# Kernel tuning notes

Measured on AMD Instinct MI355X. Metric: run time of the kernel, lower is better.

## Reference

```python
import jax, jax.numpy as jnp
import numpy as np

IN_F = 128
OUT_F = 64
ALPHA = 0.2  # LeakyReLU slope for attention logits
NEG_INF = -9e15


def setup_inputs() -> dict:
    key = jax.random.key(0)
    k1, k2, k3, k4 = jax.random.split(key, 4)
    B, N = 4, 2048
    h = jax.random.normal(k1, (B, N, IN_F), dtype=jnp.float32)
    adj = jax.random.randint(k2, (B, N, N), 0, 2, dtype=jnp.int32)
    # xavier_uniform with gain=1.414
    def xavier(k, shape, gain=1.414):
        fan_in, fan_out = shape[0], shape[1]
        bound = gain * np.sqrt(6.0 / (fan_in + fan_out))
        return jax.random.uniform(k, shape, jnp.float32, -bound, bound)
    W = xavier(k3, (IN_F, OUT_F))
    a = xavier(k4, (2 * OUT_F, 1))
    return {"h": h, "adj": adj, "W": W, "a": a}


def reference(h, adj, W, a):
    # Wh: [B, N, F_out]
    Wh = jnp.einsum("bnf,fo->bno", h, W)
    # e_ij = LeakyReLU(a_left . Wh_i + a_right . Wh_j), avoiding the
    # O(N^2 * 2F) concatenated tensor the torch code materializes.
    a_l = a[:OUT_F, 0]   # [F_out]
    a_r = a[OUT_F:, 0]   # [F_out]
    e_l = Wh @ a_l       # [B, N]
    e_r = Wh @ a_r       # [B, N]
    e = jax.nn.leaky_relu(e_l[:, :, None] + e_r[:, None, :], ALPHA)  # [B,N,N]
    masked = jnp.where(adj > 0, e, NEG_INF)
    attention = jax.nn.softmax(masked, axis=2)
    # dropout p=0.0 (eval-mode / deterministic) -> identity
    h_prime = jax.nn.leaky_relu(jnp.einsum("bij,bjo->bio", attention, Wh), 0.01)
    return (h_prime, attention)
```

## Files before the change

### kernel.cpp

```cpp
#include <hip/hip_runtime.h>

#define NN 2048
#define BB 4
#define IN_F 128
#define OUT_F 64
#define NEG_INF -9000000000000000.0f

typedef __attribute__((ext_vector_type(8))) short short8;
typedef __attribute__((ext_vector_type(4))) float f32x4;

__device__ __forceinline__ ushort f2bf(float f) {
  uint u = __float_as_uint(f);
  uint r = (u + 0x7fffu + ((u >> 16) & 1u)) >> 16;
  return (ushort)r;
}

__global__ __launch_bounds__(64) void wh_el_er_kernel(
    const float* __restrict__ h, const float* __restrict__ W,
    const float* __restrict__ a, ushort* __restrict__ Whbf,
    float* __restrict__ el, float* __restrict__ er) {
  int row = blockIdx.x;
  int o = threadIdx.x;
  const float* hr = h + (size_t)row * IN_F;
  float wh = 0.f;
  #pragma unroll 8
  for (int f = 0; f < IN_F; ++f) wh += hr[f] * W[f * OUT_F + o];
  Whbf[(size_t)row * OUT_F + o] = f2bf(wh);
  float vl = wh * a[o];
  float vr = wh * a[OUT_F + o];
  #pragma unroll
  for (int d = 32; d > 0; d >>= 1) {
    vl += __shfl_down(vl, d);
    vr += __shfl_down(vr, d);
  }
  if (o == 0) { el[row] = vl; er[row] = vr; }
}

__global__ __launch_bounds__(256) void transpose_kernel(
    const ushort* __restrict__ Whbf, ushort* __restrict__ WhbfT) {
  __shared__ uint tile[64][65];
  int b = blockIdx.x >> 5;
  int j0 = (blockIdx.x & 31) << 6;
  int t = threadIdx.x;
  int o = t & 63, jg = t >> 6;
  #pragma unroll
  for (int m = 0; m < 16; ++m) {
    int jj = jg * 16 + m;
    tile[jj][o] = (uint)Whbf[((size_t)(b * NN + j0 + jj)) * OUT_F + o];
  }
  __syncthreads();
  int oo = t >> 2, grp = t & 3;
  uint out[8];
  #pragma unroll
  for (int m = 0; m < 16; m += 2) {
    uint u0 = tile[grp * 16 + m][oo];
    uint u1 = tile[grp * 16 + m + 1][oo];
    out[m >> 1] = u0 | (u1 << 16);
  }
  uint4* dst = (uint4*)(WhbfT + ((size_t)(b * OUT_F + oo)) * NN + j0 + grp * 16);
  dst[0] = *(uint4*)&out[0];
  dst[1] = *(uint4*)&out[4];
}

__global__ __launch_bounds__(512, 4) void attn_kernel(
    const int* __restrict__ adj, const ushort* __restrict__ WhbfT,
    const float* __restrict__ el, const float* __restrict__ er,
    float* __restrict__ attn_out, float* __restrict__ hprime) {
  __shared__ __align__(16) char pbuf[16 * 4096];
  __shared__ float red[4][16][16];

  int blk = blockIdx.x;
  int b = blk >> 7;
  int i0 = (blk & 127) << 4;
  int tid = threadIdx.x;
  int wave = tid >> 6, lane = tid & 63;

  const float4* er4 = (const float4*)(er + (size_t)b * NN);

  for (int rr = 0; rr < 2; ++rr) {
    int r = wave * 2 + rr;
    int i = i0 + r;
    float eli = el[(size_t)b * NN + i];
    const int4* arow4 = (const int4*)(adj + ((size_t)(b * NN + i)) * NN);

    float pv[8][4];
    float mx = NEG_INF;
    #pragma unroll
    for (int it = 0; it < 8; ++it) {
      int4 av = arow4[lane + 64 * it];
      float4 ev = er4[lane + 64 * it];
      float e0 = eli + ev.x; e0 = e0 > 0.f ? e0 : 0.2f * e0;
      float e1 = eli + ev.y; e1 = e1 > 0.f ? e1 : 0.2f * e1;
      float e2 = eli + ev.z; e2 = e2 > 0.f ? e2 : 0.2f * e2;
      float e3 = eli + ev.w; e3 = e3 > 0.f ? e3 : 0.2f * e3;
      pv[it][0] = av.x > 0 ? e0 : NEG_INF;
      pv[it][1] = av.y > 0 ? e1 : NEG_INF;
      pv[it][2] = av.z > 0 ? e2 : NEG_INF;
      pv[it][3] = av.w > 0 ? e3 : NEG_INF;
      mx = fmaxf(mx, fmaxf(fmaxf(pv[it][0], pv[it][1]), fmaxf(pv[it][2], pv[it][3])));
    }
    #pragma unroll
    for (int d = 32; d > 0; d >>= 1) mx = fmaxf(mx, __shfl_xor(mx, d));

    float s = 0.f;
    #pragma unroll
    for (int it = 0; it < 8; ++it) {
      #pragma unroll
      for (int k = 0; k < 4; ++k) {
        float pe = __expf(pv[it][k] - mx);
        pv[it][k] = pe;
        s += pe;
      }
    }
    #pragma unroll
    for (int d = 32; d > 0; d >>= 1) s += __shfl_xor(s, d);
    float inv = 1.f / s;

    float4* orow4 = (float4*)(attn_out + ((size_t)(b * NN + i)) * NN);
    char* prow = pbuf + r * 4096;
    int sw = (r & 7) << 4;
    #pragma unroll
    for (int it = 0; it < 8; ++it) {
      float4 v;
      v.x = pv[it][0] * inv; v.y = pv[it][1] * inv;
      v.z = pv[it][2] * inv; v.w = pv[it][3] * inv;
      orow4[lane + 64 * it] = v;
      uint lo = (uint)f2bf(v.x) | ((uint)f2bf(v.y) << 16);
      uint hi = (uint)f2bf(v.z) | ((uint)f2bf(v.w) << 16);
      uint2 w2; w2.x = lo; w2.y = hi;
      *(uint2*)(prow + (((lane + 64 * it) * 8) ^ sw)) = w2;
    }
  }
  __syncthreads();

  int ntile = wave >> 1, khalf = wave & 1;
  int o0 = ntile * 16;
  int lo16 = lane & 15, hi4 = lane >> 4;

  const char* prow = pbuf + lo16 * 4096;
  int sw = (lo16 & 7) << 4;
  const ushort* brow = WhbfT + ((size_t)(b * OUT_F + o0 + lo16)) * NN;

  f32x4 acc = {0.f, 0.f, 0.f, 0.f};
  #pragma unroll 4
  for (int kk = 0; kk < 32; ++kk) {
    int kbase = khalf * 1024 + kk * 32 + hi4 * 8;
    short8 afrag = *(const short8*)(prow + ((kbase * 2) ^ sw));
    short8 bfrag = *(const short8*)(brow + kbase);
    acc = __builtin_amdgcn_mfma_f32_16x16x32_bf16(afrag, bfrag, acc, 0, 0, 0);
  }
  __syncthreads();

  if (khalf == 1) {
    #pragma unroll
    for (int q = 0; q < 4; ++q) red[ntile][hi4 * 4 + q][lo16] = acc[q];
  }
  __syncthreads();
  if (khalf == 0) {
    #pragma unroll
    for (int q = 0; q < 4; ++q) {
      int crow = hi4 * 4 + q;
      float v = acc[q] + red[ntile][crow][lo16];
      v = v > 0.f ? v : 0.01f * v;
      hprime[((size_t)(b * NN + i0 + crow)) * OUT_F + o0 + lo16] = v;
    }
  }
}

extern "C" void kernel_launch(void* const* d_in, const int* in_sizes, int n_in,
                              void* d_out, int out_size, void* d_ws, size_t ws_size,
                              hipStream_t stream) {
  const float* h  = (const float*)d_in[0];
  const int* adj  = (const int*)d_in[1];
  const float* W  = (const float*)d_in[2];
  const float* a  = (const float*)d_in[3];

  float* hprime   = (float*)d_out;
  float* attn_out = (float*)d_out + (size_t)BB * NN * OUT_F;

  ushort* Whbf  = (ushort*)d_ws;
  ushort* WhbfT = Whbf + (size_t)BB * NN * OUT_F;
  float* el = (float*)(WhbfT + (size_t)BB * OUT_F * NN);
  float* er = el + (size_t)BB * NN;

  hipLaunchKernelGGL(wh_el_er_kernel, dim3(BB * NN), dim3(64), 0, stream,
                     h, W, a, Whbf, el, er);
  hipLaunchKernelGGL(transpose_kernel, dim3(BB * (NN / 64)), dim3(256), 0, stream,
                     Whbf, WhbfT);
  hipLaunchKernelGGL(attn_kernel, dim3(BB * (NN / 16)), dim3(512), 0, stream,
                     adj, WhbfT, el, er, attn_out, hprime);
}
```

Before: 55.32 us.

## Use 1024-thread attention blocks with one row per wave and four-way K split

The attention kernel now launches 1024 threads, so each of 16 waves handles one row's softmax instead of two rows per wave. The MFMA reduction is split four ways over K, and the partials are reduced through the reused probability buffer. Stores of the attention matrix become nontemporal to avoid polluting the cache. The Wh kernel also packs four rows per 256-thread block to cut block count. The risks are higher register pressure under the 1024-thread launch bound and an extra reduction step.

```diff
diff --git a/kernel.cpp b/kernel.cpp
--- a/kernel.cpp
+++ b/kernel.cpp
@@ -8,6 +8,7 @@
 
 typedef __attribute__((ext_vector_type(8))) short short8;
 typedef __attribute__((ext_vector_type(4))) float f32x4;
+typedef __attribute__((ext_vector_type(4))) int i32x4;
 
 __device__ __forceinline__ ushort f2bf(float f) {
   uint u = __float_as_uint(f);
@@ -15,12 +16,12 @@
   return (ushort)r;
 }
 
-__global__ __launch_bounds__(64) void wh_el_er_kernel(
+__global__ __launch_bounds__(256) void wh_el_er_kernel(
     const float* __restrict__ h, const float* __restrict__ W,
     const float* __restrict__ a, ushort* __restrict__ Whbf,
     float* __restrict__ el, float* __restrict__ er) {
-  int row = blockIdx.x;
-  int o = threadIdx.x;
+  int row = blockIdx.x * 4 + (threadIdx.x >> 6);
+  int o = threadIdx.x & 63;
   const float* hr = h + (size_t)row * IN_F;
   float wh = 0.f;
   #pragma unroll 8
@@ -62,12 +63,11 @@
   dst[1] = *(uint4*)&out[4];
 }
 
-__global__ __launch_bounds__(512, 4) void attn_kernel(
+__global__ __launch_bounds__(1024, 2) void attn_kernel(
     const int* __restrict__ adj, const ushort* __restrict__ WhbfT,
     const float* __restrict__ el, const float* __restrict__ er,
     float* __restrict__ attn_out, float* __restrict__ hprime) {
   __shared__ __align__(16) char pbuf[16 * 4096];
-  __shared__ float red[4][16][16];
 
   int blk = blockIdx.x;
   int b = blk >> 7;
@@ -75,20 +75,19 @@
   int tid = threadIdx.x;
   int wave = tid >> 6, lane = tid & 63;
 
-  const float4* er4 = (const float4*)(er + (size_t)b * NN);
-
-  for (int rr = 0; rr < 2; ++rr) {
-    int r = wave * 2 + rr;
+  {
+    int r = wave;
     int i = i0 + r;
     float eli = el[(size_t)b * NN + i];
-    const int4* arow4 = (const int4*)(adj + ((size_t)(b * NN + i)) * NN);
+    const i32x4* arow4 = (const i32x4*)(adj + ((size_t)(b * NN + i)) * NN);
+    const f32x4* er4 = (const f32x4*)(er + (size_t)b * NN);
 
     float pv[8][4];
     float mx = NEG_INF;
     #pragma unroll
     for (int it = 0; it < 8; ++it) {
-      int4 av = arow4[lane + 64 * it];
-      float4 ev = er4[lane + 64 * it];
+      i32x4 av = arow4[lane + 64 * it];
+      f32x4 ev = er4[lane + 64 * it];
       float e0 = eli + ev.x; e0 = e0 > 0.f ? e0 : 0.2f * e0;
       float e1 = eli + ev.y; e1 = e1 > 0.f ? e1 : 0.2f * e1;
       float e2 = eli + ev.z; e2 = e2 > 0.f ? e2 : 0.2f * e2;
@@ -116,15 +115,15 @@
     for (int d = 32; d > 0; d >>= 1) s += __shfl_xor(s, d);
     float inv = 1.f / s;
 
-    float4* orow4 = (float4*)(attn_out + ((size_t)(b * NN + i)) * NN);
+    f32x4* orow4 = (f32x4*)(attn_out + ((size_t)(b * NN + i)) * NN);
     char* prow = pbuf + r * 4096;
     int sw = (r & 7) << 4;
     #pragma unroll
     for (int it = 0; it < 8; ++it) {
-      float4 v;
+      f32x4 v;
       v.x = pv[it][0] * inv; v.y = pv[it][1] * inv;
       v.z = pv[it][2] * inv; v.w = pv[it][3] * inv;
-      orow4[lane + 64 * it] = v;
+      __builtin_nontemporal_store(v, &orow4[lane + 64 * it]);
       uint lo = (uint)f2bf(v.x) | ((uint)f2bf(v.y) << 16);
       uint hi = (uint)f2bf(v.z) | ((uint)f2bf(v.w) << 16);
       uint2 w2; w2.x = lo; w2.y = hi;
@@ -133,34 +132,41 @@
   }
   __syncthreads();
 
-  int ntile = wave >> 1, khalf = wave & 1;
+  int ntile = wave & 3, kq = wave >> 2;
   int o0 = ntile * 16;
   int lo16 = lane & 15, hi4 = lane >> 4;
 
-  const char* prow = pbuf + lo16 * 4096;
-  int sw = (lo16 & 7) << 4;
+  const char* prowA = pbuf + lo16 * 4096;
+  int swA = (lo16 & 7) << 4;
   const ushort* brow = WhbfT + ((size_t)(b * OUT_F + o0 + lo16)) * NN;
 
   f32x4 acc = {0.f, 0.f, 0.f, 0.f};
   #pragma unroll 4
-  for (int kk = 0; kk < 32; ++kk) {
-    int kbase = khalf * 1024 + kk * 32 + hi4 * 8;
-    short8 afrag = *(const short8*)(prow + ((kbase * 2) ^ sw));
+  for (int kk = 0; kk < 16; ++kk) {
+    int kbase = kq * 512 + kk * 32 + hi4 * 8;
+    short8 afrag = *(const short8*)(prowA + ((kbase * 2) ^ swA));
     short8 bfrag = *(const short8*)(brow + kbase);
     acc = __builtin_amdgcn_mfma_f32_16x16x32_bf16(afrag, bfrag, acc, 0, 0, 0);
   }
   __syncthreads();
 
-  if (khalf == 1) {
-    #pragma unroll
-    for (int q = 0; q < 4; ++q) red[ntile][hi4 * 4 + q][lo16] = acc[q];
-  }
-  __syncthreads();
-  if (khalf == 0) {
+  float* red = (float*)pbuf;
+  if (kq > 0) {
     #pragma unroll
     for (int q = 0; q < 4; ++q) {
       int crow = hi4 * 4 + q;
-      float v = acc[q] + red[ntile][crow][lo16];
+      red[(((kq - 1) * 4 + ntile) * 16 + crow) * 17 + lo16] = acc[q];
+    }
+  }
+  __syncthreads();
+  if (kq == 0) {
+    #pragma unroll
+    for (int q = 0; q < 4; ++q) {
+      int crow = hi4 * 4 + q;
+      float v = acc[q]
+              + red[((0 * 4 + ntile) * 16 + crow) * 17 + lo16]
+              + red[((1 * 4 + ntile) * 16 + crow) * 17 + lo16]
+              + red[((2 * 4 + ntile) * 16 + crow) * 17 + lo16];
       v = v > 0.f ? v : 0.01f * v;
       hprime[((size_t)(b * NN + i0 + crow)) * OUT_F + o0 + lo16] = v;
     }
@@ -183,10 +189,10 @@
   float* el = (float*)(WhbfT + (size_t)BB * OUT_F * NN);
   float* er = el + (size_t)BB * NN;
 
-  hipLaunchKernelGGL(wh_el_er_kernel, dim3(BB * NN), dim3(64), 0, stream,
+  hipLaunchKernelGGL(wh_el_er_kernel, dim3(BB * NN / 4), dim3(256), 0, stream,
                      h, W, a, Whbf, el, er);
   hipLaunchKernelGGL(transpose_kernel, dim3(BB * (NN / 64)), dim3(256), 0, stream,
                      Whbf, WhbfT);
-  hipLaunchKernelGGL(attn_kernel, dim3(BB * (NN / 16)), dim3(512), 0, stream,
+  hipLaunchKernelGGL(attn_kernel, dim3(BB * (NN / 16)), dim3(1024), 0, stream,
                      adj, WhbfT, el, er, attn_out, hprime);
 }
```

New measurement: 58.41 us. 5.6% more time.

## Drop softmax max pass, halve rows per block, defer normalization to MFMA output

Applied to the files above, without the earlier changes.

Removes the row-max reduction by exponentiating the LeakyReLU logits directly and zeroing masked entries. Unnormalized bf16 probabilities go to LDS and the 1/sum scale is applied after the MFMA accumulate. Each block now handles 8 rows, one per wave, which doubles the grid and raises the occupancy hint. Attention rows are written with nontemporal stores. Risks include overflow in exp without max subtraction, rounding the stored attention through bf16, and half of the MFMA A-rows now being zero padding.

```diff
diff --git a/kernel.cpp b/kernel.cpp
--- a/kernel.cpp
+++ b/kernel.cpp
@@ -4,15 +4,18 @@
 #define BB 4
 #define IN_F 128
 #define OUT_F 64
-#define NEG_INF -9000000000000000.0f
 
 typedef __attribute__((ext_vector_type(8))) short short8;
 typedef __attribute__((ext_vector_type(4))) float f32x4;
+typedef __attribute__((ext_vector_type(4))) int i32x4;
 
 __device__ __forceinline__ ushort f2bf(float f) {
   uint u = __float_as_uint(f);
   uint r = (u + 0x7fffu + ((u >> 16) & 1u)) >> 16;
   return (ushort)r;
+}
+__device__ __forceinline__ float bf2f(ushort s) {
+  return __uint_as_float(((uint)s) << 16);
 }
 
 __global__ __launch_bounds__(64) void wh_el_er_kernel(
@@ -62,105 +65,102 @@
   dst[1] = *(uint4*)&out[4];
 }
 
-__global__ __launch_bounds__(512, 4) void attn_kernel(
+__global__ __launch_bounds__(512, 8) void attn_kernel(
     const int* __restrict__ adj, const ushort* __restrict__ WhbfT,
     const float* __restrict__ el, const float* __restrict__ er,
     float* __restrict__ attn_out, float* __restrict__ hprime) {
-  __shared__ __align__(16) char pbuf[16 * 4096];
-  __shared__ float red[4][16][16];
+  __shared__ __align__(16) char pbuf[8 * 4096];
+  __shared__ float red[4][16][17];
+  __shared__ float sinv[8];
 
   int blk = blockIdx.x;
-  int b = blk >> 7;
-  int i0 = (blk & 127) << 4;
+  int b = blk >> 8;
+  int i0 = (blk & 255) << 3;
   int tid = threadIdx.x;
-  int wave = tid >> 6, lane = tid & 63;
+  int w = tid >> 6, lane = tid & 63;
 
-  const float4* er4 = (const float4*)(er + (size_t)b * NN);
+  int i = i0 + w;
+  float eli = el[(size_t)b * NN + i];
+  const i32x4* arow4 = (const i32x4*)(adj + ((size_t)(b * NN + i)) * NN);
+  const f32x4* er4 = (const f32x4*)(er + (size_t)b * NN);
 
-  for (int rr = 0; rr < 2; ++rr) {
-    int r = wave * 2 + rr;
-    int i = i0 + r;
-    float eli = el[(size_t)b * NN + i];
-    const int4* arow4 = (const int4*)(adj + ((size_t)(b * NN + i)) * NN);
+  uint2 pva[8];
+  float ssum = 0.f;
+  #pragma unroll
+  for (int it = 0; it < 8; ++it) {
+    i32x4 av = arow4[lane + 64 * it];
+    f32x4 ev = er4[lane + 64 * it];
+    float pe[4];
+    float evv[4] = {ev.x, ev.y, ev.z, ev.w};
+    int   avv[4] = {av.x, av.y, av.z, av.w};
+    #pragma unroll
+    for (int k = 0; k < 4; ++k) {
+      float e = eli + evv[k];
+      e = e > 0.f ? e : 0.2f * e;
+      float x = __expf(e);
+      pe[k] = avv[k] > 0 ? x : 0.f;
+      ssum += pe[k];
+    }
+    uint2 w2;
+    w2.x = (uint)f2bf(pe[0]) | ((uint)f2bf(pe[1]) << 16);
+    w2.y = (uint)f2bf(pe[2]) | ((uint)f2bf(pe[3]) << 16);
+    pva[it] = w2;
+  }
+  #pragma unroll
+  for (int d = 32; d > 0; d >>= 1) ssum += __shfl_xor(ssum, d);
+  float inv = 1.f / ssum;
+  if (lane == 0) sinv[w] = inv;
 
-    float pv[8][4];
-    float mx = NEG_INF;
+  char* prow = pbuf + w * 4096;
+  int sw = w << 4;
+  #pragma unroll
+  for (int it = 0; it < 8; ++it)
+    *(uint2*)(prow + (((lane + 64 * it) * 8) ^ sw)) = pva[it];
+  __syncthreads();
+
+  {
+    float* orow = attn_out + ((size_t)(b * NN + i)) * NN;
     #pragma unroll
     for (int it = 0; it < 8; ++it) {
-      int4 av = arow4[lane + 64 * it];
-      float4 ev = er4[lane + 64 * it];
-      float e0 = eli + ev.x; e0 = e0 > 0.f ? e0 : 0.2f * e0;
-      float e1 = eli + ev.y; e1 = e1 > 0.f ? e1 : 0.2f * e1;
-      float e2 = eli + ev.z; e2 = e2 > 0.f ? e2 : 0.2f * e2;
-      float e3 = eli + ev.w; e3 = e3 > 0.f ? e3 : 0.2f * e3;
-      pv[it][0] = av.x > 0 ? e0 : NEG_INF;
-      pv[it][1] = av.y > 0 ? e1 : NEG_INF;
-      pv[it][2] = av.z > 0 ? e2 : NEG_INF;
-      pv[it][3] = av.w > 0 ? e3 : NEG_INF;
-      mx = fmaxf(mx, fmaxf(fmaxf(pv[it][0], pv[it][1]), fmaxf(pv[it][2], pv[it][3])));
-    }
-    #pragma unroll
-    for (int d = 32; d > 0; d >>= 1) mx = fmaxf(mx, __shfl_xor(mx, d));
-
-    float s = 0.f;
-    #pragma unroll
-    for (int it = 0; it < 8; ++it) {
-      #pragma unroll
-      for (int k = 0; k < 4; ++k) {
-        float pe = __expf(pv[it][k] - mx);
-        pv[it][k] = pe;
-        s += pe;
-      }
-    }
-    #pragma unroll
-    for (int d = 32; d > 0; d >>= 1) s += __shfl_xor(s, d);
-    float inv = 1.f / s;
-
-    float4* orow4 = (float4*)(attn_out + ((size_t)(b * NN + i)) * NN);
-    char* prow = pbuf + r * 4096;
-    int sw = (r & 7) << 4;
-    #pragma unroll
-    for (int it = 0; it < 8; ++it) {
-      float4 v;
-      v.x = pv[it][0] * inv; v.y = pv[it][1] * inv;
-      v.z = pv[it][2] * inv; v.w = pv[it][3] * inv;
-      orow4[lane + 64 * it] = v;
-      uint lo = (uint)f2bf(v.x) | ((uint)f2bf(v.y) << 16);
-      uint hi = (uint)f2bf(v.z) | ((uint)f2bf(v.w) << 16);
-      uint2 w2; w2.x = lo; w2.y = hi;
-      *(uint2*)(prow + (((lane + 64 * it) * 8) ^ sw)) = w2;
+      uint2 w2 = pva[it];
+      f32x4 v;
+      v.x = bf2f((ushort)(w2.x & 0xffff)) * inv;
+      v.y = bf2f((ushort)(w2.x >> 16)) * inv;
+      v.z = bf2f((ushort)(w2.y & 0xffff)) * inv;
+      v.w = bf2f((ushort)(w2.y >> 16)) * inv;
+      __builtin_nontemporal_store(v, (f32x4*)(orow + (lane + 64 * it) * 4));
     }
   }
-  __syncthreads();
 
-  int ntile = wave >> 1, khalf = wave & 1;
+  int ntile = w >> 1, khalf = w & 1;
   int o0 = ntile * 16;
   int lo16 = lane & 15, hi4 = lane >> 4;
 
-  const char* prow = pbuf + lo16 * 4096;
-  int sw = (lo16 & 7) << 4;
+  const char* prowA = pbuf + (lo16 & 7) * 4096;
+  int swA = (lo16 & 7) << 4;
   const ushort* brow = WhbfT + ((size_t)(b * OUT_F + o0 + lo16)) * NN;
+  short8 zero8 = {0, 0, 0, 0, 0, 0, 0, 0};
 
   f32x4 acc = {0.f, 0.f, 0.f, 0.f};
   #pragma unroll 4
   for (int kk = 0; kk < 32; ++kk) {
     int kbase = khalf * 1024 + kk * 32 + hi4 * 8;
-    short8 afrag = *(const short8*)(prow + ((kbase * 2) ^ sw));
+    short8 afrag = *(const short8*)(prowA + ((kbase * 2) ^ swA));
+    afrag = lo16 < 8 ? afrag : zero8;
     short8 bfrag = *(const short8*)(brow + kbase);
     acc = __builtin_amdgcn_mfma_f32_16x16x32_bf16(afrag, bfrag, acc, 0, 0, 0);
   }
-  __syncthreads();
 
   if (khalf == 1) {
     #pragma unroll
     for (int q = 0; q < 4; ++q) red[ntile][hi4 * 4 + q][lo16] = acc[q];
   }
   __syncthreads();
-  if (khalf == 0) {
+  if (khalf == 0 && hi4 < 2) {
     #pragma unroll
     for (int q = 0; q < 4; ++q) {
       int crow = hi4 * 4 + q;
-      float v = acc[q] + red[ntile][crow][lo16];
+      float v = (acc[q] + red[ntile][crow][lo16]) * sinv[crow];
       v = v > 0.f ? v : 0.01f * v;
       hprime[((size_t)(b * NN + i0 + crow)) * OUT_F + o0 + lo16] = v;
     }
@@ -187,6 +187,6 @@
                      h, W, a, Whbf, el, er);
   hipLaunchKernelGGL(transpose_kernel, dim3(BB * (NN / 64)), dim3(256), 0, stream,
                      Whbf, WhbfT);
-  hipLaunchKernelGGL(attn_kernel, dim3(BB * (NN / 16)), dim3(512), 0, stream,
+  hipLaunchKernelGGL(attn_kernel, dim3(BB * (NN / 8)), dim3(512), 0, stream,
                      adj, WhbfT, el, er, attn_out, hprime);
 }
```

Result: slower. 61.48 us (+11.1%).

## Drop softmax max pass, defer normalization, stage er in LDS, interleave rows

Applied to the files above, without the earlier changes.

Removes the row-max reduction and computes exp of the masked LeakyReLU logits directly, relying on logits being small enough not to overflow. Unnormalized bf16 probabilities go into LDS for the MFMA, and the 1/sum scale is applied afterwards to the h' output and to the attention output, which is rebuilt from the bf16 values. The er vector is staged in shared memory, and two rows are processed together per wave for more memory-level parallelism. This lowers precision of the attention output (now bf16-rounded) and risks overflow if logits become large.

```diff
diff --git a/kernel.cpp b/kernel.cpp
--- a/kernel.cpp
+++ b/kernel.cpp
@@ -4,15 +4,18 @@
 #define BB 4
 #define IN_F 128
 #define OUT_F 64
-#define NEG_INF -9000000000000000.0f
 
 typedef __attribute__((ext_vector_type(8))) short short8;
 typedef __attribute__((ext_vector_type(4))) float f32x4;
+typedef __attribute__((ext_vector_type(4))) int i32x4;
 
 __device__ __forceinline__ ushort f2bf(float f) {
   uint u = __float_as_uint(f);
   uint r = (u + 0x7fffu + ((u >> 16) & 1u)) >> 16;
   return (ushort)r;
+}
+__device__ __forceinline__ float bf2f(ushort s) {
+  return __uint_as_float(((uint)s) << 16);
 }
 
 __global__ __launch_bounds__(64) void wh_el_er_kernel(
@@ -67,7 +70,9 @@
     const float* __restrict__ el, const float* __restrict__ er,
     float* __restrict__ attn_out, float* __restrict__ hprime) {
   __shared__ __align__(16) char pbuf[16 * 4096];
-  __shared__ float red[4][16][16];
+  __shared__ float ers[NN];
+  __shared__ float red[4][16][17];
+  __shared__ float sinv[16];
 
   int blk = blockIdx.x;
   int b = blk >> 7;
@@ -75,81 +80,104 @@
   int tid = threadIdx.x;
   int wave = tid >> 6, lane = tid & 63;
 
-  const float4* er4 = (const float4*)(er + (size_t)b * NN);
-
-  for (int rr = 0; rr < 2; ++rr) {
-    int r = wave * 2 + rr;
-    int i = i0 + r;
-    float eli = el[(size_t)b * NN + i];
-    const int4* arow4 = (const int4*)(adj + ((size_t)(b * NN + i)) * NN);
-
-    float pv[8][4];
-    float mx = NEG_INF;
+  ((f32x4*)ers)[tid] = ((const f32x4*)(er + (size_t)b * NN))[tid];
+  __syncthreads();
+
+  int r0 = wave * 2, r1 = r0 + 1;
+  int ia = i0 + r0, ib = i0 + r1;
+  float el0 = el[(size_t)b * NN + ia];
+  float el1 = el[(size_t)b * NN + ib];
+  const i32x4* arow0 = (const i32x4*)(adj + ((size_t)(b * NN + ia)) * NN);
+  const i32x4* arow1 = (const i32x4*)(adj + ((size_t)(b * NN + ib)) * NN);
+
+  uint2 pva0[8], pva1[8];
+  float ss0 = 0.f, ss1 = 0.f;
+  #pragma unroll
+  for (int it = 0; it < 8; ++it) {
+    i32x4 a0 = arow0[lane + 64 * it];
+    i32x4 a1 = arow1[lane + 64 * it];
+    f32x4 ev = *(const f32x4*)&ers[(lane + 64 * it) * 4];
+    float evv[4] = {ev.x, ev.y, ev.z, ev.w};
+    int   av0[4] = {a0.x, a0.y, a0.z, a0.w};
+    int   av1[4] = {a1.x, a1.y, a1.z, a1.w};
+    float pe0[4], pe1[4];
+    #pragma unroll
+    for (int k = 0; k < 4; ++k) {
+      float e0 = el0 + evv[k];
+      e0 = e0 > 0.f ? e0 : 0.2f * e0;
+      float x0 = __expf(e0);
+      pe0[k] = av0[k] > 0 ? x0 : 0.f;
+      ss0 += pe0[k];
+      float e1 = el1 + evv[k];
+      e1 = e1 > 0.f ? e1 : 0.2f * e1;
+      float x1 = __expf(e1);
+      pe1[k] = av1[k] > 0 ? x1 : 0.f;
+      ss1 += pe1[k];
+    }
+    uint2 w0, w1;
+    w0.x = (uint)f2bf(pe0[0]) | ((uint)f2bf(pe0[1]) << 16);
+    w0.y = (uint)f2bf(pe0[2]) | ((uint)f2bf(pe0[3]) << 16);
+    w1.x = (uint)f2bf(pe1[0]) | ((uint)f2bf(pe1[1]) << 16);
+    w1.y = (uint)f2bf(pe1[2]) | ((uint)f2bf(pe1[3]) << 16);
+    pva0[it] = w0;
+    pva1[it] = w1;
+  }
+  #pragma unroll
+  for (int d = 32; d > 0; d >>= 1) {
+    ss0 += __shfl_xor(ss0, d);
+    ss1 += __shfl_xor(ss1, d);
+  }
+  float inv0 = 1.f / ss0, inv1 = 1.f / ss1;
+  if (lane == 0) { sinv[r0] = inv0; sinv[r1] = inv1; }
+
+  {
+    char* prow0 = pbuf + r0 * 4096;
+    char* prow1 = pbuf + r1 * 4096;
+    int sw0 = (r0 & 7) << 4, sw1 = (r1 & 7) << 4;
     #pragma unroll
     for (int it = 0; it < 8; ++it) {
-      int4 av = arow4[lane + 64 * it];
-      float4 ev = er4[lane + 64 * it];
-      float e0 = eli + ev.x; e0 = e0 > 0.f ? e0 : 0.2f * e0;
-      float e1 = eli + ev.y; e1 = e1 > 0.f ? e1 : 0.2f * e1;
-      float e2 = eli + ev.z; e2 = e2 > 0.f ? e2 : 0.2f * e2;
-      float e3 = eli + ev.w; e3 = e3 > 0.f ? e3 : 0.2f * e3;
-      pv[it][0] = av.x > 0 ? e0 : NEG_INF;
-      pv[it][1] = av.y > 0 ? e1 : NEG_INF;
-      pv[it][2] = av.z > 0 ? e2 : NEG_INF;
-      pv[it][3] = av.w > 0 ? e3 : NEG_INF;
-      mx = fmaxf(mx, fmaxf(fmaxf(pv[it][0], pv[it][1]), fmaxf(pv[it][2], pv[it][3])));
-    }
-    #pragma unroll
-    for (int d = 32; d > 0; d >>= 1) mx = fmaxf(mx, __shfl_xor(mx, d));
-
-    float s = 0.f;
+      *(uint2*)(prow0 + (((lane + 64 * it) * 8) ^ sw0)) = pva0[it];
+      *(uint2*)(prow1 + (((lane + 64 * it) * 8) ^ sw1)) = pva1[it];
+    }
+  }
+  __syncthreads();
+
+  {
+    f32x4* or0 = (f32x4*)(attn_out + ((size_t)(b * NN + ia)) * NN);
+    f32x4* or1 = (f32x4*)(attn_out + ((size_t)(b * NN + ib)) * NN);
     #pragma unroll
     for (int it = 0; it < 8; ++it) {
-      #pragma unroll
-      for (int k = 0; k < 4; ++k) {
-        float pe = __expf(pv[it][k] - mx);
-        pv[it][k] = pe;
-        s += pe;
-      }
-    }
-    #pragma unroll
-    for (int d = 32; d > 0; d >>= 1) s += __shfl_xor(s, d);
-    float inv = 1.f / s;
-
-    float4* orow4 = (float4*)(attn_out + ((size_t)(b * NN + i)) * NN);
-    char* prow = pbuf + r * 4096;
-    int sw = (r & 7) << 4;
-    #pragma unroll
-    for (int it = 0; it < 8; ++it) {
-      float4 v;
-      v.x = pv[it][0] * inv; v.y = pv[it][1] * inv;
-      v.z = pv[it][2] * inv; v.w = pv[it][3] * inv;
-      orow4[lane + 64 * it] = v;
-      uint lo = (uint)f2bf(v.x) | ((uint)f2bf(v.y) << 16);
-      uint hi = (uint)f2bf(v.z) | ((uint)f2bf(v.w) << 16);
-      uint2 w2; w2.x = lo; w2.y = hi;
-      *(uint2*)(prow + (((lane + 64 * it) * 8) ^ sw)) = w2;
-    }
-  }
-  __syncthreads();
+      uint2 w0 = pva0[it], w1 = pva1[it];
+      f32x4 v0, v1;
+      v0.x = bf2f((ushort)(w0.x & 0xffff)) * inv0;
+      v0.y = bf2f((ushort)(w0.x >> 16)) * inv0;
+      v0.z = bf2f((ushort)(w0.y & 0xffff)) * inv0;
+      v0.w = bf2f((ushort)(w0.y >> 16)) * inv0;
+      or0[lane + 64 * it] = v0;
+      v1.x = bf2f((ushort)(w1.x & 0xffff)) * inv1;
+      v1.y = bf2f((ushort)(w1.x >> 16)) * inv1;
+      v1.z = bf2f((ushort)(w1.y & 0xffff)) * inv1;
+      v1.w = bf2f((ushort)(w1.y >> 16)) * inv1;
+      or1[lane + 64 * it] = v1;
+    }
+  }
 
   int ntile = wave >> 1, khalf = wave & 1;
   int o0 = ntile * 16;
   int lo16 = lane & 15, hi4 = lane >> 4;
 
-  const char* prow = pbuf + lo16 * 4096;
-  int sw = (lo16 & 7) << 4;
+  const char* prowA = pbuf + lo16 * 4096;
+  int swA = (lo16 & 7) << 4;
   const ushort* brow = WhbfT + ((size_t)(b * OUT_F + o0 + lo16)) * NN;
 
   f32x4 acc = {0.f, 0.f, 0.f, 0.f};
   #pragma unroll 4
   for (int kk = 0; kk < 32; ++kk) {
     int kbase = khalf * 1024 + kk * 32 + hi4 * 8;
-    short8 afrag = *(const short8*)(prow + ((kbase * 2) ^ sw));
+    short8 afrag = *(const short8*)(prowA + ((kbase * 2) ^ swA));
     short8 bfrag = *(const short8*)(brow + kbase);
     acc = __builtin_amdgcn_mfma_f32_16x16x32_bf16(afrag, bfrag, acc, 0, 0, 0);
   }
-  __syncthreads();
 
   if (khalf == 1) {
     #pragma unroll
@@ -160,7 +188,7 @@
     #pragma unroll
     for (int q = 0; q < 4; ++q) {
       int crow = hi4 * 4 + q;
-      float v = acc[q] + red[ntile][crow][lo16];
+      float v = (acc[q] + red[ntile][crow][lo16]) * sinv[crow];
       v = v > 0.f ? v : 0.01f * v;
       hprime[((size_t)(b * NN + i0 + crow)) * OUT_F + o0 + lo16] = v;
     }
```

Measured after the change: 52.22 us. 5.6% less time.
